# Performance work log

Measured on AMD Instinct MI355X. Metric: run time of the kernel, lower is better.

## Reference

```python
import jax, jax.numpy as jnp
import numpy as np

EMBED_DIM = 256
NUM_CLASSES = 100000
BATCH = 1024
MARGIN = 0.2
SCALE = 30.0
EPS = 1e-07


def setup_inputs() -> dict:
    key = jax.random.key(0)
    k1, k2, k3 = jax.random.split(key, 3)
    embeddings = jax.random.normal(k1, (BATCH, EMBED_DIM), dtype=jnp.float32)
    # xavier_normal_ init for weight [num_classes, embed_dim]
    std = float(np.sqrt(2.0 / (NUM_CLASSES + EMBED_DIM)))
    weight = jax.random.normal(k2, (NUM_CLASSES, EMBED_DIM), dtype=jnp.float32) * std
    labels = jax.random.randint(k3, (BATCH,), 0, NUM_CLASSES, dtype=jnp.int64)
    return {"embeddings": embeddings, "weight": weight, "labels": labels}


def _l2_normalize(x, axis):
    # matches F.normalize(dim=..) with default eps=1e-12
    norm = jnp.linalg.norm(x, axis=axis, keepdims=True)
    return x / jnp.maximum(norm, 1e-12)


def reference(embeddings, weight, labels):
    emb_n = _l2_normalize(embeddings, axis=1)          # [B, D]
    w_n = _l2_normalize(weight, axis=1)                # [C, D]
    cos_theta = jnp.clip(emb_n @ w_n.T, -1.0 + EPS, 1.0 - EPS)  # [B, C]
    theta = jnp.arccos(cos_theta)
    target_mask = jax.nn.one_hot(labels, NUM_CLASSES, dtype=jnp.bool_)
    theta_m = jnp.where(target_mask, theta + MARGIN, theta)
    logits = SCALE * jnp.cos(theta_m)                  # [B, C]
    logp = jax.nn.log_softmax(logits, axis=1)
    loss = -jnp.mean(jnp.take_along_axis(logp, labels[:, None], axis=1))
    acc = jnp.mean((jnp.argmax(logits, axis=1) == labels).astype(jnp.float32))
    return (loss, acc)
```

## Files before the change

### kernel.cpp

```cpp
#include <hip/hip_runtime.h>
#include <stdint.h>

#define DIM    256
#define BATCH  1024
#define NCLS   100000
#define NCT    256
#define TPG    25
#define CPG    (TPG * 16)
#define NCLS_PAD (NCT * CPG)
#define RG     8
#define CLIPV  0.9999999f
#define COSM   0.98006657784124163f
#define SINM   0.19866933079506122f
#define K30L2E 43.280851226668903f

typedef __attribute__((ext_vector_type(4))) float floatx4;
typedef __attribute__((ext_vector_type(2))) unsigned long ulong2v;

#define EMBF_OFF 0
#define WGTF_OFF (256 * 1024)
#define TL_OFF   (WGTF_OFF + (size_t)NCLS_PAD * DIM)
#define PU_OFF   (TL_OFF + 4096)
#define SP_OFF   (PU_OFF + 4096)
#define MP_OFF   (SP_OFF + (size_t)NCT * BATCH * 4)

__global__ __launch_bounds__(256) void k_norm8f(
        const float* __restrict__ src, unsigned char* __restrict__ dst,
        int nvalid) {
    const int tid = threadIdx.x;
    const int w = tid >> 6, l = tid & 63;
    const int r   = blockIdx.x * 16 + w * 4 + (l >> 4);
    const int r16 = r & 15;
    const int l16 = l & 15;
    float v[16];
    float ss = 0.f;
    if (r < nvalid) {
        const float* rp = src + (size_t)r * DIM + l16 * 16;
#pragma unroll
        for (int i = 0; i < 4; ++i) {
            float4 a = *(const float4*)(rp + i * 4);
            v[i*4+0]=a.x; v[i*4+1]=a.y; v[i*4+2]=a.z; v[i*4+3]=a.w;
            ss += a.x*a.x + a.y*a.y + a.z*a.z + a.w*a.w;
        }
    } else {
#pragma unroll
        for (int i = 0; i < 16; ++i) v[i] = 0.f;
    }
#pragma unroll
    for (int k = 1; k < 16; k <<= 1) ss += __shfl_xor(ss, k);
    const float sc = 1.f / fmaxf(sqrtf(ss), 1e-12f);
    unsigned char* tb = dst + (size_t)(r >> 4) * 4096;
#pragma unroll
    for (int h = 0; h < 2; ++h) {
        const int g = 2 * l16 + h;
        const int s = g >> 2, q = g & 3;
        int p0 = 0, p1 = 0;
        p0 = __builtin_amdgcn_cvt_pk_fp8_f32(v[h*8+0]*sc, v[h*8+1]*sc, p0, false);
        p0 = __builtin_amdgcn_cvt_pk_fp8_f32(v[h*8+2]*sc, v[h*8+3]*sc, p0, true);
        p1 = __builtin_amdgcn_cvt_pk_fp8_f32(v[h*8+4]*sc, v[h*8+5]*sc, p1, false);
        p1 = __builtin_amdgcn_cvt_pk_fp8_f32(v[h*8+6]*sc, v[h*8+7]*sc, p1, true);
        uint2 o; o.x = (unsigned)p0; o.y = (unsigned)p1;
        *(uint2*)(tb + (s >> 1) * 1024 + (r16 + 16 * q) * 16 + (s & 1) * 8) = o;
    }
}

__global__ __launch_bounds__(256) void k_target(
        const float* __restrict__ emb, const float* __restrict__ wgt,
        const int* __restrict__ labels,
        float* __restrict__ TL, float* __restrict__ PU) {
    const int tid = threadIdx.x;
    const int w = tid >> 6, l = tid & 63;
    const int r   = blockIdx.x * 16 + w * 4 + (l >> 4);
    const int l16 = l & 15;
    const int lbl = labels[r];
    const float* ep = emb + (size_t)r * DIM + l16 * 16;
    const float* wp = wgt + (size_t)lbl * DIM + l16 * 16;
    float de = 0.f, dw = 0.f, dd = 0.f;
#pragma unroll
    for (int i = 0; i < 4; ++i) {
        float4 a = *(const float4*)(ep + i * 4);
        float4 b = *(const float4*)(wp + i * 4);
        de += a.x*a.x + a.y*a.y + a.z*a.z + a.w*a.w;
        dw += b.x*b.x + b.y*b.y + b.z*b.z + b.w*b.w;
        dd += a.x*b.x + a.y*b.y + a.z*b.z + a.w*b.w;
    }
#pragma unroll
    for (int k = 1; k < 16; k <<= 1) {
        de += __shfl_xor(de, k); dw += __shfl_xor(dw, k); dd += __shfl_xor(dd, k);
    }
    if (l16 == 0) {
        float t = dd / (fmaxf(sqrtf(de), 1e-12f) * fmaxf(sqrtf(dw), 1e-12f));
        t = fminf(fmaxf(t, -CLIPV), CLIPV);
        PU[r] = exp2f(fmaf(t, K30L2E, -K30L2E));
        TL[r] = t * COSM - sqrtf(fmaxf(1.f - t * t, 0.f)) * SINM;
    }
}

__global__ __launch_bounds__(256, 6) void k_main(
        const unsigned char* __restrict__ wgt8f,
        const unsigned char* __restrict__ emb8f,
        float* __restrict__ SP, unsigned* __restrict__ MP) {
    const int cg = blockIdx.x;
    const int rg = blockIdx.y;
    const int tid = threadIdx.x;
    const int w = tid >> 6, l = tid & 63;
    const int r16 = l & 15, q = l >> 4;
    const int rowbase = rg * 128 + w * 32;

    long af[2][8];
#pragma unroll
    for (int mt = 0; mt < 2; ++mt) {
        const ulong2v* ap =
            (const ulong2v*)(emb8f + (size_t)((rowbase >> 4) + mt) * 4096) + l;
#pragma unroll
        for (int p = 0; p < 4; ++p) {
            ulong2v v = ap[p * 64];
            af[mt][2*p]   = (long)v.x;
            af[mt][2*p+1] = (long)v.y;
        }
    }

    float sum[2][4] = {{0.f,0.f,0.f,0.f},{0.f,0.f,0.f,0.f}};
    float mx [2][4] = {{0.f,0.f,0.f,0.f},{0.f,0.f,0.f,0.f}};

    const ulong2v* bp = (const ulong2v*)(wgt8f + (size_t)(cg * TPG) * 4096) + l;
    for (int t = 0; t < TPG; ++t, bp += 256) {
        long bf[8];
#pragma unroll
        for (int p = 0; p < 4; ++p) {
            ulong2v v = bp[p * 64];
            bf[2*p]   = (long)v.x;
            bf[2*p+1] = (long)v.y;
        }
#pragma unroll
        for (int mt = 0; mt < 2; ++mt) {
            floatx4 acc = {0.f, 0.f, 0.f, 0.f};
#pragma unroll
            for (int s = 0; s < 8; ++s)
                acc = __builtin_amdgcn_mfma_f32_16x16x32_fp8_fp8(af[mt][s], bf[s], acc, 0, 0, 0);
#pragma unroll
            for (int r = 0; r < 4; ++r) {
                const float p = exp2f(fmaf(acc[r], K30L2E, -K30L2E));
                sum[mt][r] += p;
                mx[mt][r] = fmaxf(mx[mt][r], p);
            }
        }
    }

#pragma unroll
    for (int k = 1; k < 16; k <<= 1)
#pragma unroll
        for (int mt = 0; mt < 2; ++mt)
#pragma unroll
            for (int r = 0; r < 4; ++r) {
                sum[mt][r] += __shfl_xor(sum[mt][r], k);
                mx[mt][r] = fmaxf(mx[mt][r], __shfl_xor(mx[mt][r], k));
            }
    if (r16 < 4) {
#pragma unroll
        for (int mt = 0; mt < 2; ++mt) {
            float sv = sum[mt][0], mv = mx[mt][0];
            if (r16 == 1) { sv = sum[mt][1]; mv = mx[mt][1]; }
            else if (r16 == 2) { sv = sum[mt][2]; mv = mx[mt][2]; }
            else if (r16 == 3) { sv = sum[mt][3]; mv = mx[mt][3]; }
            const int row = rowbase + mt * 16 + q * 4 + r16;
            SP[cg * BATCH + row] = sv;
            MP[cg * BATCH + row] = __float_as_uint(mv);
        }
    }
}

__global__ __launch_bounds__(256) void k_final(
        const float* __restrict__ SP, const unsigned* __restrict__ MP,
        const float* __restrict__ TL, const float* __restrict__ PU,
        float* __restrict__ out) {
    __shared__ float    ls[16][16];
    __shared__ unsigned lm[16][16];
    const int tid = threadIdx.x;
    const int r16 = tid & 15;
    const int c   = tid >> 4;
    const int row = blockIdx.x * 16 + r16;
    float s = 0.f;
    unsigned m = 0u;
    for (int b = c; b < NCT; b += 16) {
        s += SP[(size_t)b * BATCH + row];
        const unsigned v = MP[(size_t)b * BATCH + row];
        m = v > m ? v : m;
    }
    ls[c][r16] = s; lm[c][r16] = m;
    __syncthreads();
    float loss = 0.f, corr = 0.f;
    if (tid < 16) {
        float st = 0.f; unsigned mt = 0u;
#pragma unroll
        for (int i = 0; i < 16; ++i) {
            st += ls[i][tid];
            mt = lm[i][tid] > mt ? lm[i][tid] : mt;
        }
        const int r = blockIdx.x * 16 + tid;
        const float tl = TL[r];
        const float padj = exp2f(fmaf(tl, K30L2E, -K30L2E));
        st = st - PU[r] + padj;
        loss = 30.f + logf(st) - 30.f * tl;
        corr = (padj >= __uint_as_float(mt)) ? 1.f : 0.f;
    }
#pragma unroll
    for (int k = 1; k < 16; k <<= 1) {
        loss += __shfl_xor(loss, k);
        corr += __shfl_xor(corr, k);
    }
    if (tid == 0) {
        atomicAdd(out + 0, loss * (1.f / 1024.f));
        atomicAdd(out + 1, corr * (1.f / 1024.f));
    }
}

extern "C" void kernel_launch(void* const* d_in, const int* in_sizes, int n_in,
                              void* d_out, int out_size, void* d_ws, size_t ws_size,
                              hipStream_t stream) {
    (void)in_sizes; (void)n_in; (void)out_size; (void)ws_size;
    const float* emb    = (const float*)d_in[0];
    const float* wgt    = (const float*)d_in[1];
    const int*   labels = (const int*)d_in[2];
    char* ws = (char*)d_ws;
    unsigned char* emb8f = (unsigned char*)(ws + EMBF_OFF);
    unsigned char* wgt8f = (unsigned char*)(ws + WGTF_OFF);
    float*    TL = (float*)(ws + TL_OFF);
    float*    PU = (float*)(ws + PU_OFF);
    float*    SP = (float*)(ws + SP_OFF);
    unsigned* MP = (unsigned*)(ws + MP_OFF);

    hipMemsetAsync(d_out, 0, 2 * sizeof(float), stream);
    k_norm8f<<<BATCH / 16, 256, 0, stream>>>(emb, emb8f, BATCH);
    k_norm8f<<<NCLS_PAD / 16, 256, 0, stream>>>(wgt, wgt8f, NCLS);
    k_target<<<BATCH / 16, 256, 0, stream>>>(emb, wgt, labels, TL, PU);
    k_main<<<dim3(NCT, RG), 256, 0, stream>>>(wgt8f, emb8f, SP, MP);
    k_final<<<64, 256, 0, stream>>>(SP, MP, TL, PU, (float*)d_out);
}
```

Baseline: 220.5 us.

## Fuse prep kernels, drop class padding, fold softmax scale into fp8 operands

Merges the two normalize/quantize launches and the target-logit kernel into one launch with block-range dispatch. Class padding is removed (250 tiles of 400 classes exactly cover 100000), so no zero rows are quantized or multiplied. Both operands are prescaled by sqrt(30*log2e) so the MFMA result feeds exp2 directly, which removes the per-element FMA and the constant shift. The trade is that exp2 now runs without the max offset and the fp8 values carry a larger scale, which could affect range and rounding.

```diff
diff --git a/kernel.cpp b/kernel.cpp
--- a/kernel.cpp
+++ b/kernel.cpp
@@ -4,37 +4,46 @@
 #define DIM    256
 #define BATCH  1024
 #define NCLS   100000
-#define NCT    256
+#define NCT    250
 #define TPG    25
-#define CPG    (TPG * 16)
-#define NCLS_PAD (NCT * CPG)
+#define CPG    400
 #define RG     8
+#define WGTBLK 6250
 #define CLIPV  0.9999999f
 #define COSM   0.98006657784124163f
 #define SINM   0.19866933079506122f
 #define K30L2E 43.280851226668903f
+#define SQK    6.5788184f
 
 typedef __attribute__((ext_vector_type(4))) float floatx4;
 typedef __attribute__((ext_vector_type(2))) unsigned long ulong2v;
 
 #define EMBF_OFF 0
 #define WGTF_OFF (256 * 1024)
-#define TL_OFF   (WGTF_OFF + (size_t)NCLS_PAD * DIM)
+#define TL_OFF   (WGTF_OFF + (size_t)NCLS * DIM)
 #define PU_OFF   (TL_OFF + 4096)
 #define SP_OFF   (PU_OFF + 4096)
 #define MP_OFF   (SP_OFF + (size_t)NCT * BATCH * 4)
 
-__global__ __launch_bounds__(256) void k_norm8f(
-        const float* __restrict__ src, unsigned char* __restrict__ dst,
-        int nvalid) {
+__global__ __launch_bounds__(256) void k_prep(
+        const float* __restrict__ emb, const float* __restrict__ wgt,
+        const int* __restrict__ labels,
+        unsigned char* __restrict__ emb8f, unsigned char* __restrict__ wgt8f,
+        float* __restrict__ TL, float* __restrict__ PU) {
+    const int b = blockIdx.x;
     const int tid = threadIdx.x;
     const int w = tid >> 6, l = tid & 63;
-    const int r   = blockIdx.x * 16 + w * 4 + (l >> 4);
-    const int r16 = r & 15;
+    const int sub = w * 4 + (l >> 4);
     const int l16 = l & 15;
-    float v[16];
-    float ss = 0.f;
-    if (r < nvalid) {
+
+    if (b < 64 + WGTBLK) {
+        const bool isEmb = (b < 64);
+        const float* src = isEmb ? emb : wgt;
+        unsigned char* dst = isEmb ? emb8f : wgt8f;
+        const int r = (isEmb ? b : b - 64) * 16 + sub;
+        const int r16 = r & 15;
+        float v[16];
+        float ss = 0.f;
         const float* rp = src + (size_t)r * DIM + l16 * 16;
 #pragma unroll
         for (int i = 0; i < 4; ++i) {
@@ -42,57 +51,46 @@
             v[i*4+0]=a.x; v[i*4+1]=a.y; v[i*4+2]=a.z; v[i*4+3]=a.w;
             ss += a.x*a.x + a.y*a.y + a.z*a.z + a.w*a.w;
         }
+#pragma unroll
+        for (int k = 1; k < 16; k <<= 1) ss += __shfl_xor(ss, k);
+        const float sc = SQK / fmaxf(sqrtf(ss), 1e-12f);
+        unsigned char* tb = dst + (size_t)(r >> 4) * 4096;
+#pragma unroll
+        for (int h = 0; h < 2; ++h) {
+            const int g = 2 * l16 + h;
+            const int s = g >> 2, q = g & 3;
+            int p0 = 0, p1 = 0;
+            p0 = __builtin_amdgcn_cvt_pk_fp8_f32(v[h*8+0]*sc, v[h*8+1]*sc, p0, false);
+            p0 = __builtin_amdgcn_cvt_pk_fp8_f32(v[h*8+2]*sc, v[h*8+3]*sc, p0, true);
+            p1 = __builtin_amdgcn_cvt_pk_fp8_f32(v[h*8+4]*sc, v[h*8+5]*sc, p1, false);
+            p1 = __builtin_amdgcn_cvt_pk_fp8_f32(v[h*8+6]*sc, v[h*8+7]*sc, p1, true);
+            uint2 o; o.x = (unsigned)p0; o.y = (unsigned)p1;
+            *(uint2*)(tb + (s >> 1) * 1024 + (r16 + 16 * q) * 16 + (s & 1) * 8) = o;
+        }
     } else {
-#pragma unroll
-        for (int i = 0; i < 16; ++i) v[i] = 0.f;
-    }
-#pragma unroll
-    for (int k = 1; k < 16; k <<= 1) ss += __shfl_xor(ss, k);
-    const float sc = 1.f / fmaxf(sqrtf(ss), 1e-12f);
-    unsigned char* tb = dst + (size_t)(r >> 4) * 4096;
-#pragma unroll
-    for (int h = 0; h < 2; ++h) {
-        const int g = 2 * l16 + h;
-        const int s = g >> 2, q = g & 3;
-        int p0 = 0, p1 = 0;
-        p0 = __builtin_amdgcn_cvt_pk_fp8_f32(v[h*8+0]*sc, v[h*8+1]*sc, p0, false);
-        p0 = __builtin_amdgcn_cvt_pk_fp8_f32(v[h*8+2]*sc, v[h*8+3]*sc, p0, true);
-        p1 = __builtin_amdgcn_cvt_pk_fp8_f32(v[h*8+4]*sc, v[h*8+5]*sc, p1, false);
-        p1 = __builtin_amdgcn_cvt_pk_fp8_f32(v[h*8+6]*sc, v[h*8+7]*sc, p1, true);
-        uint2 o; o.x = (unsigned)p0; o.y = (unsigned)p1;
-        *(uint2*)(tb + (s >> 1) * 1024 + (r16 + 16 * q) * 16 + (s & 1) * 8) = o;
-    }
-}
-
-__global__ __launch_bounds__(256) void k_target(
-        const float* __restrict__ emb, const float* __restrict__ wgt,
-        const int* __restrict__ labels,
-        float* __restrict__ TL, float* __restrict__ PU) {
-    const int tid = threadIdx.x;
-    const int w = tid >> 6, l = tid & 63;
-    const int r   = blockIdx.x * 16 + w * 4 + (l >> 4);
-    const int l16 = l & 15;
-    const int lbl = labels[r];
-    const float* ep = emb + (size_t)r * DIM + l16 * 16;
-    const float* wp = wgt + (size_t)lbl * DIM + l16 * 16;
-    float de = 0.f, dw = 0.f, dd = 0.f;
-#pragma unroll
-    for (int i = 0; i < 4; ++i) {
-        float4 a = *(const float4*)(ep + i * 4);
-        float4 b = *(const float4*)(wp + i * 4);
-        de += a.x*a.x + a.y*a.y + a.z*a.z + a.w*a.w;
-        dw += b.x*b.x + b.y*b.y + b.z*b.z + b.w*b.w;
-        dd += a.x*b.x + a.y*b.y + a.z*b.z + a.w*b.w;
-    }
-#pragma unroll
-    for (int k = 1; k < 16; k <<= 1) {
-        de += __shfl_xor(de, k); dw += __shfl_xor(dw, k); dd += __shfl_xor(dd, k);
-    }
-    if (l16 == 0) {
-        float t = dd / (fmaxf(sqrtf(de), 1e-12f) * fmaxf(sqrtf(dw), 1e-12f));
-        t = fminf(fmaxf(t, -CLIPV), CLIPV);
-        PU[r] = exp2f(fmaf(t, K30L2E, -K30L2E));
-        TL[r] = t * COSM - sqrtf(fmaxf(1.f - t * t, 0.f)) * SINM;
+        const int r = (b - 64 - WGTBLK) * 16 + sub;
+        const int lbl = labels[r];
+        const float* ep = emb + (size_t)r * DIM + l16 * 16;
+        const float* wp = wgt + (size_t)lbl * DIM + l16 * 16;
+        float de = 0.f, dw = 0.f, dd = 0.f;
+#pragma unroll
+        for (int i = 0; i < 4; ++i) {
+            float4 a = *(const float4*)(ep + i * 4);
+            float4 bq = *(const float4*)(wp + i * 4);
+            de += a.x*a.x + a.y*a.y + a.z*a.z + a.w*a.w;
+            dw += bq.x*bq.x + bq.y*bq.y + bq.z*bq.z + bq.w*bq.w;
+            dd += a.x*bq.x + a.y*bq.y + a.z*bq.z + a.w*bq.w;
+        }
+#pragma unroll
+        for (int k = 1; k < 16; k <<= 1) {
+            de += __shfl_xor(de, k); dw += __shfl_xor(dw, k); dd += __shfl_xor(dd, k);
+        }
+        if (l16 == 0) {
+            float t = dd / (fmaxf(sqrtf(de), 1e-12f) * fmaxf(sqrtf(dw), 1e-12f));
+            t = fminf(fmaxf(t, -CLIPV), CLIPV);
+            PU[r] = exp2f(t * K30L2E);
+            TL[r] = t * COSM - sqrtf(fmaxf(1.f - t * t, 0.f)) * SINM;
+        }
     }
 }
 
@@ -140,7 +138,7 @@
                 acc = __builtin_amdgcn_mfma_f32_16x16x32_fp8_fp8(af[mt][s], bf[s], acc, 0, 0, 0);
 #pragma unroll
             for (int r = 0; r < 4; ++r) {
-                const float p = exp2f(fmaf(acc[r], K30L2E, -K30L2E));
+                const float p = exp2f(acc[r]);
                 sum[mt][r] += p;
                 mx[mt][r] = fmaxf(mx[mt][r], p);
             }
@@ -199,9 +197,9 @@
         }
         const int r = blockIdx.x * 16 + tid;
         const float tl = TL[r];
-        const float padj = exp2f(fmaf(tl, K30L2E, -K30L2E));
+        const float padj = exp2f(tl * K30L2E);
         st = st - PU[r] + padj;
-        loss = 30.f + logf(st) - 30.f * tl;
+        loss = logf(st) - 30.f * tl;
         corr = (padj >= __uint_as_float(mt)) ? 1.f : 0.f;
     }
 #pragma unroll
@@ -231,9 +229,8 @@
     unsigned* MP = (unsigned*)(ws + MP_OFF);
 
     hipMemsetAsync(d_out, 0, 2 * sizeof(float), stream);
-    k_norm8f<<<BATCH / 16, 256, 0, stream>>>(emb, emb8f, BATCH);
-    k_norm8f<<<NCLS_PAD / 16, 256, 0, stream>>>(wgt, wgt8f, NCLS);
-    k_target<<<BATCH / 16, 256, 0, stream>>>(emb, wgt, labels, TL, PU);
+    k_prep<<<64 + WGTBLK + 64, 256, 0, stream>>>(emb, wgt, labels,
+                                                 emb8f, wgt8f, TL, PU);
     k_main<<<dim3(NCT, RG), 256, 0, stream>>>(wgt8f, emb8f, SP, MP);
     k_final<<<64, 256, 0, stream>>>(SP, MP, TL, PU, (float*)d_out);
 }
```

Result: no change. 218.2 us (-1.0%).
